# Performance work log

Measured on AMD Instinct MI355X. Metric: run time of the kernel, lower is better.

Reference implementation:

```python
import jax, jax.numpy as jnp
import numpy as np

B, I, H1, H2, E, T = 16384, 512, 256, 128, 8, 2


def setup_inputs() -> dict:
    key = jax.random.key(0)
    ks = jax.random.split(key, 4)
    # Xavier-ish scaling for stability
    x = jax.random.normal(ks[0], (B, I), dtype=jnp.float32)
    W1 = jax.random.normal(ks[1], (E, I, H1), dtype=jnp.float32) / np.sqrt(I)
    b1 = jnp.zeros((E, H1), dtype=jnp.float32)
    W2 = jax.random.normal(ks[2], (E, H1, H2), dtype=jnp.float32) / np.sqrt(H1)
    b2 = jnp.zeros((E, H2), dtype=jnp.float32)
    Wg = jax.random.normal(ks[3], (T, I, E), dtype=jnp.float32) / np.sqrt(I)
    bg = jnp.zeros((T, E), dtype=jnp.float32)
    return {"x": x, "W1": W1, "b1": b1, "W2": W2, "b2": b2, "Wg": Wg, "bg": bg}


def reference(x, W1, b1, W2, b2, Wg, bg):
    # All experts as one grouped GEMM: [E, B, H1]
    h = jax.nn.relu(jnp.einsum('bi,eih->ebh', x, W1) + b1[:, None, :])
    # Last expert layer (lastlayer_reg=True -> act applied): [E, B, H2]
    e_out = jax.nn.relu(jnp.einsum('ebh,eho->ebo', h, W2) + b2[:, None, :])
    # Per-task gates with softmax over experts: [T, B, E]
    gates = jax.nn.softmax(jnp.einsum('bi,tie->tbe', x, Wg) + bg[:, None, :], axis=-1)
    # Gate-weighted combine of expert outputs: [T, B, H2]
    towers = jnp.einsum('tbe,ebo->tbo', gates, e_out)
    return towers
```

## Files before the change

### kernel.cpp

```cpp
#include <hip/hip_runtime.h>
#include <hip/hip_bf16.h>

#define B_  16384
#define I_  512
#define H1_ 256
#define H2_ 128
#define E_  8
#define T_  2

typedef __attribute__((ext_vector_type(8))) short short8;
typedef __attribute__((ext_vector_type(4))) float float4_t;

__device__ inline unsigned short f2bf(float f) {
    union { float f; unsigned u; } v; v.f = f;
    unsigned r = v.u + 0x7FFFu + ((v.u >> 16) & 1u);
    return (unsigned short)(r >> 16);
}

__device__ inline void async_copy16(const unsigned short* g, unsigned short* l) {
    __builtin_amdgcn_global_load_lds(
        (const __attribute__((address_space(1))) void*)g,
        (__attribute__((address_space(3))) void*)l,
        16, 0, 0);
}

__global__ void prep_gates_kernel(const float* __restrict__ x,
                                  unsigned short* __restrict__ xb,
                                  const float* __restrict__ W1,
                                  unsigned short* __restrict__ w1t,
                                  const float* __restrict__ W2,
                                  unsigned short* __restrict__ w2t,
                                  const float* __restrict__ Wg,
                                  const float* __restrict__ bg,
                                  float* __restrict__ gates) {
    __shared__ __align__(16) char smem[16 * 520 * 2 + 4 * 16 * 16 * 4];
    int bid = blockIdx.x;
    int t = threadIdx.x;

    if (bid < 1024) {
        unsigned short* wgtL = (unsigned short*)smem;
        float (*red)[16][16] = (float (*)[16][16])(smem + 16 * 520 * 2);
#pragma unroll
        for (int j = 0; j < 32; ++j) {
            int idx = j * 256 + t;
            int e = idx & 7, i = (idx >> 3) & 511, task = idx >> 12;
            wgtL[(task * 8 + e) * 520 + i] = f2bf(Wg[idx]);
        }
        __syncthreads();

        int w = t >> 6, lane = t & 63;
        int col = lane & 15, quad = lane >> 4;
        int b0 = bid * 16;
        int k0 = w * 128;
        const float* xr = x + (size_t)(b0 + col) * I_ + k0 + quad * 8;
        unsigned short* xw = xb + (size_t)(b0 + col) * I_ + k0 + quad * 8;
        const unsigned short* bL = &wgtL[col * 520 + k0 + quad * 8];
        float4_t acc = {0.f, 0.f, 0.f, 0.f};
#pragma unroll
        for (int ks = 0; ks < 128; ks += 32) {
            float4_t xa = *(const float4_t*)(xr + ks);
            float4_t xc = *(const float4_t*)(xr + ks + 4);
            short8 a;
            a[0] = (short)f2bf(xa[0]); a[1] = (short)f2bf(xa[1]);
            a[2] = (short)f2bf(xa[2]); a[3] = (short)f2bf(xa[3]);
            a[4] = (short)f2bf(xc[0]); a[5] = (short)f2bf(xc[1]);
            a[6] = (short)f2bf(xc[2]); a[7] = (short)f2bf(xc[3]);
            *(short8*)(xw + ks) = a;
            short8 b = *(const short8*)(bL + ks);
            acc = __builtin_amdgcn_mfma_f32_16x16x32_bf16(a, b, acc, 0, 0, 0);
        }
#pragma unroll
        for (int p = 0; p < 4; ++p)
            red[w][quad * 4 + p][col] = acc[p];
        __syncthreads();
        int r = t >> 4, te = t & 15;
        float v = red[0][r][te] + red[1][r][te] + red[2][r][te] + red[3][r][te] + bg[te];
        float m = v;
        m = fmaxf(m, __shfl_xor(m, 1));
        m = fmaxf(m, __shfl_xor(m, 2));
        m = fmaxf(m, __shfl_xor(m, 4));
        float ev = __expf(v - m);
        float s = ev;
        s += __shfl_xor(s, 1);
        s += __shfl_xor(s, 2);
        s += __shfl_xor(s, 4);
        gates[(size_t)te * B_ + b0 + r] = ev / s;
    } else {
        float (*tile)[33] = (float (*)[33])smem;
        const float* in; unsigned short* outp; int R, C, e, r0, c0;
        if (bid < 2048) {
            int tl = bid - 1024;
            e = tl >> 7; int rem = tl & 127;
            R = I_; C = H1_;
            r0 = (rem >> 3) * 32; c0 = (rem & 7) * 32;
            in = W1; outp = w1t;
        } else {
            int tl = bid - 2048;
            e = tl >> 5; int rem = tl & 31;
            R = H1_; C = H2_;
            r0 = (rem >> 2) * 32; c0 = (rem & 3) * 32;
            in = W2; outp = w2t;
        }
        const float* inp = in + (size_t)e * R * C;
        unsigned short* op = outp + (size_t)e * R * C;
        int tx = t & 31, ty = t >> 5;
#pragma unroll
        for (int j = 0; j < 32; j += 8)
            tile[ty + j][tx] = inp[(size_t)(r0 + ty + j) * C + c0 + tx];
        __syncthreads();
#pragma unroll
        for (int j = 0; j < 32; j += 8)
            op[(size_t)(c0 + ty + j) * R + r0 + tx] = f2bf(tile[tx][ty + j]);
    }
}

__global__ __launch_bounds__(512, 2)
void l1_gemm_kernel(const unsigned short* __restrict__ xb,
                    const unsigned short* __restrict__ w1t,
                    const float* __restrict__ b1,
                    unsigned short* __restrict__ h) {
    __shared__ __align__(16) unsigned short smem[65536];

    int bid = blockIdx.x;
    int wg = (bid & 7) * 64 + (bid >> 3);
    int m0 = (wg >> 3) * 256;
    int e  = wg & 7;

    int t = threadIdx.x, w = t >> 6, lane = t & 63;
    int col = lane & 15, quad = lane >> 4;
    int wm = (w & 1) * 128;
    int wn = (w >> 1) * 64;

    int rowA = t >> 3;
    int csw  = ((t & 7) ^ (rowA & 7)) * 8;
    const unsigned short* aG = xb  + (size_t)(m0 + rowA) * I_ + csw;
    const unsigned short* bG = w1t + ((size_t)e * H1_ + rowA) * I_ + csw;

    unsigned short* As = smem;
    unsigned short* Bs = smem + 32768;
    int ldsw = w * 512;

    float4_t acc[8][4];
#pragma unroll
    for (int mf = 0; mf < 8; ++mf)
#pragma unroll
        for (int nf = 0; nf < 4; ++nf)
            acc[mf][nf] = (float4_t){0.f, 0.f, 0.f, 0.f};

#pragma unroll
    for (int p = 0; p < 4; ++p) {
        async_copy16(aG + ((size_t)p * 64) * I_, As + p * 4096 + ldsw);
        async_copy16(bG + ((size_t)p * 64) * I_, Bs + p * 4096 + ldsw);
    }

#pragma unroll 1
    for (int kt = 0; kt < 8; ++kt) {
        const int cur = kt & 1;
        const unsigned short* Ac = As + cur * 16384;
        const unsigned short* Bc = Bs + cur * 16384;

        if (kt < 7) {
            unsigned short* An = As + (cur ^ 1) * 16384;
            unsigned short* Bn = Bs + (cur ^ 1) * 16384;
            const unsigned short* aN = aG + (size_t)(kt + 1) * 64;
            const unsigned short* bN = bG + (size_t)(kt + 1) * 64;
#pragma unroll
            for (int p = 0; p < 4; ++p) {
                async_copy16(aN + ((size_t)p * 64) * I_, An + p * 4096 + ldsw);
                async_copy16(bN + ((size_t)p * 64) * I_, Bn + p * 4096 + ldsw);
            }
            asm volatile("s_waitcnt vmcnt(8)" ::: "memory");
        } else {
            asm volatile("s_waitcnt vmcnt(0)" ::: "memory");
        }
        asm volatile("s_barrier" ::: "memory");

#pragma unroll
        for (int kq = 0; kq < 2; ++kq) {
            int q = kq * 4 + quad;
            short8 af[8], bfv[4];
#pragma unroll
            for (int mf = 0; mf < 8; ++mf) {
                int r = wm + mf * 16 + col;
                af[mf] = *(const short8*)&Ac[r * 64 + ((q ^ (r & 7)) << 3)];
            }
#pragma unroll
            for (int nf = 0; nf < 4; ++nf) {
                int n = wn + nf * 16 + col;
                bfv[nf] = *(const short8*)&Bc[n * 64 + ((q ^ (n & 7)) << 3)];
            }
            __builtin_amdgcn_s_setprio(1);
#pragma unroll
            for (int mf = 0; mf < 8; ++mf)
#pragma unroll
                for (int nf = 0; nf < 4; ++nf)
                    acc[mf][nf] = __builtin_amdgcn_mfma_f32_16x16x32_bf16(
                        af[mf], bfv[nf], acc[mf][nf], 0, 0, 0);
            __builtin_amdgcn_s_setprio(0);
        }
        asm volatile("s_barrier" ::: "memory");
    }

    unsigned short* Ct = smem;
    const float* bE = b1 + e * H1_;
#pragma unroll
    for (int half = 0; half < 2; ++half) {
        if ((w & 1) == half) {
#pragma unroll
            for (int mf = 0; mf < 8; ++mf) {
#pragma unroll
                for (int nf = 0; nf < 4; ++nf) {
                    int n = wn + nf * 16 + col;
                    float bv = bE[n];
#pragma unroll
                    for (int p2 = 0; p2 < 4; ++p2) {
                        float v = acc[mf][nf][p2] + bv;
                        v = v > 0.f ? v : 0.f;
                        Ct[(mf * 16 + quad * 4 + p2) * 264 + n] = f2bf(v);
                    }
                }
            }
        }
        __syncthreads();
        unsigned short* hrow = h + ((size_t)e * B_ + m0 + half * 128) * H1_;
#pragma unroll
        for (int j = 0; j < 8; ++j) {
            int idx = j * 512 + t;
            int row = idx >> 5, cc = idx & 31;
            short8 vv = *(const short8*)&Ct[row * 264 + cc * 8];
            *(short8*)&hrow[(size_t)row * H1_ + cc * 8] = vv;
        }
        __syncthreads();
    }
}

__global__ __launch_bounds__(512, 4)
void fused_l2_combine_kernel(const unsigned short* __restrict__ h,
                             const unsigned short* __restrict__ w2t,
                             const float* __restrict__ b2,
                             const float* __restrict__ gates,
                             float* __restrict__ out) {
    __shared__ __align__(16) unsigned short ring[36864];
    __shared__ float gL[16][64];

    unsigned short* Aslot = ring;
    unsigned short* Bslot = ring + 12288;

    int b0 = blockIdx.x * 64;
    int t = threadIdx.x, w = t >> 6, lane = t & 63;
    int col = lane & 15, quad = lane >> 4;
    int wm = (w & 1) * 32, wn = (w >> 1) * 32;

    if (t < 256) {
        int te = t >> 4, r4 = (t & 15) * 4;
        *(float4_t*)&gL[te][r4] = *(const float4_t*)&gates[(size_t)te * B_ + b0 + r4];
    }

    int rowA = t >> 3;
    int csw  = ((t & 7) ^ (rowA & 7)) * 8;
    int ldsw = w * 512;

    float4_t tw0[2][2], tw1[2][2];
#pragma unroll
    for (int mi = 0; mi < 2; ++mi)
#pragma unroll
        for (int ni = 0; ni < 2; ++ni) {
            tw0[mi][ni] = (float4_t){0.f, 0.f, 0.f, 0.f};
            tw1[mi][ni] = (float4_t){0.f, 0.f, 0.f, 0.f};
        }

    auto stage = [&](int cid, int slot) {
        int ee = cid >> 2, kc = cid & 3;
        const unsigned short* hE = h + ((size_t)ee * B_ + b0 + rowA) * H1_ + kc * 64 + csw;
        async_copy16(hE, Aslot + slot * 4096 + ldsw);
        const unsigned short* wE = w2t + ((size_t)ee * H2_ + rowA) * H1_ + kc * 64 + csw;
        async_copy16(wE, Bslot + slot * 8192 + ldsw);
        async_copy16(wE + (size_t)64 * H1_, Bslot + slot * 8192 + 4096 + ldsw);
    };

    stage(0, 0);

    float4_t acc[2][2];
    int rd = 0, wr = 1;
#pragma unroll 1
    for (int cid = 0; cid < 32; ++cid) {
        if (cid < 31) {
            stage(cid + 1, wr);
            asm volatile("s_waitcnt vmcnt(3)" ::: "memory");
        } else {
            asm volatile("s_waitcnt vmcnt(0)" ::: "memory");
        }
        asm volatile("s_barrier" ::: "memory");

        if ((cid & 3) == 0) {
#pragma unroll
            for (int mi = 0; mi < 2; ++mi)
#pragma unroll
                for (int ni = 0; ni < 2; ++ni)
                    acc[mi][ni] = (float4_t){0.f, 0.f, 0.f, 0.f};
        }
        const unsigned short* Ac = Aslot + rd * 4096;
        const unsigned short* Bc = Bslot + rd * 8192;
#pragma unroll
        for (int kq = 0; kq < 2; ++kq) {
            int q = kq * 4 + quad;
            short8 af[2], bfv[2];
#pragma unroll
            for (int mi = 0; mi < 2; ++mi) {
                int r = wm + mi * 16 + col;
                af[mi] = *(const short8*)&Ac[r * 64 + ((q ^ (r & 7)) << 3)];
            }
#pragma unroll
            for (int ni = 0; ni < 2; ++ni) {
                int n = wn + ni * 16 + col;
                bfv[ni] = *(const short8*)&Bc[n * 64 + ((q ^ (n & 7)) << 3)];
            }
            __builtin_amdgcn_s_setprio(1);
#pragma unroll
            for (int mi = 0; mi < 2; ++mi)
#pragma unroll
                for (int ni = 0; ni < 2; ++ni)
                    acc[mi][ni] = __builtin_amdgcn_mfma_f32_16x16x32_bf16(
                        af[mi], bfv[ni], acc[mi][ni], 0, 0, 0);
            __builtin_amdgcn_s_setprio(0);
        }

        if ((cid & 3) == 3) {
            int ee = cid >> 2;
#pragma unroll
            for (int ni = 0; ni < 2; ++ni) {
                float bv = b2[ee * H2_ + wn + ni * 16 + col];
#pragma unroll
                for (int mi = 0; mi < 2; ++mi) {
#pragma unroll
                    for (int p = 0; p < 4; ++p) {
                        int rloc = wm + mi * 16 + quad * 4 + p;
                        float v = acc[mi][ni][p] + bv;
                        v = v > 0.f ? v : 0.f;
                        tw0[mi][ni][p] += gL[ee][rloc] * v;
                        tw1[mi][ni][p] += gL[8 + ee][rloc] * v;
                    }
                }
            }
        }
        rd = (rd == 2) ? 0 : rd + 1;
        wr = (wr == 2) ? 0 : wr + 1;
    }

#pragma unroll
    for (int mi = 0; mi < 2; ++mi) {
#pragma unroll
        for (int ni = 0; ni < 2; ++ni) {
            int n = wn + ni * 16 + col;
#pragma unroll
            for (int p = 0; p < 4; ++p) {
                int r = b0 + wm + mi * 16 + quad * 4 + p;
                out[(size_t)r * H2_ + n] = tw0[mi][ni][p];
                out[(size_t)B_ * H2_ + (size_t)r * H2_ + n] = tw1[mi][ni][p];
            }
        }
    }
}

extern "C" void kernel_launch(void* const* d_in, const int* in_sizes, int n_in,
                              void* d_out, int out_size, void* d_ws, size_t ws_size,
                              hipStream_t stream) {
    const float* x  = (const float*)d_in[0];
    const float* W1 = (const float*)d_in[1];
    const float* b1 = (const float*)d_in[2];
    const float* W2 = (const float*)d_in[3];
    const float* b2 = (const float*)d_in[4];
    const float* Wg = (const float*)d_in[5];
    const float* bg = (const float*)d_in[6];
    float* out = (float*)d_out;

    char* ws = (char*)d_ws;
    unsigned short* xb    = (unsigned short*)(ws);
    unsigned short* w1t   = (unsigned short*)(ws + 16777216);
    unsigned short* w2t   = (unsigned short*)(ws + 18874368);
    float*          gates = (float*)(ws + 19398656);
    unsigned short* h     = (unsigned short*)(ws + 20447232);

    prep_gates_kernel<<<dim3(2304), 256, 0, stream>>>(x, xb, W1, w1t, W2, w2t, Wg, bg, gates);

    l1_gemm_kernel<<<dim3(512), 512, 0, stream>>>(xb, w1t, b1, h);

    fused_l2_combine_kernel<<<dim3(B_ / 64), 512, 0, stream>>>(h, w2t, b2, gates, out);
}
```

Before: 163.6 us.

## Restructure L1 GEMM main loop into quadrant-level ping-pong pipeline

```diff
diff --git a/kernel.cpp b/kernel.cpp
--- a/kernel.cpp
+++ b/kernel.cpp
@@ -23,6 +23,10 @@
         (__attribute__((address_space(3))) void*)l,
         16, 0, 0);
 }
+
+#define BAR()  asm volatile("s_barrier" ::: "memory")
+#define LGKM() do { asm volatile("s_waitcnt lgkmcnt(0)" ::: "memory"); \
+                    __builtin_amdgcn_sched_barrier(0); } while (0)
 
 __global__ void prep_gates_kernel(const float* __restrict__ x,
                                   unsigned short* __restrict__ xb,
@@ -131,14 +135,10 @@
     int wm = (w & 1) * 128;
     int wn = (w >> 1) * 64;
 
-    int rowA = t >> 3;
-    int csw  = ((t & 7) ^ (rowA & 7)) * 8;
-    const unsigned short* aG = xb  + (size_t)(m0 + rowA) * I_ + csw;
-    const unsigned short* bG = w1t + ((size_t)e * H1_ + rowA) * I_ + csw;
+    int cswT = ((t & 7) ^ ((t >> 3) & 7)) * 8;
 
     unsigned short* As = smem;
     unsigned short* Bs = smem + 32768;
-    int ldsw = w * 512;
 
     float4_t acc[8][4];
 #pragma unroll
@@ -147,58 +147,102 @@
         for (int nf = 0; nf < 4; ++nf)
             acc[mf][nf] = (float4_t){0.f, 0.f, 0.f, 0.f};
 
-#pragma unroll
-    for (int p = 0; p < 4; ++p) {
-        async_copy16(aG + ((size_t)p * 64) * I_, As + p * 4096 + ldsw);
-        async_copy16(bG + ((size_t)p * 64) * I_, Bs + p * 4096 + ldsw);
-    }
+    auto stageA = [&](int kt, int mq, int bsel) {
+#pragma unroll
+        for (int hh = 0; hh < 2; ++hh) {
+            int lr = mq * 128 + hh * 64 + (t >> 3);
+            int m  = ((lr >> 6) & 1) * 128 + ((lr >> 7) & 1) * 64 + (lr & 63);
+            async_copy16(xb + (size_t)(m0 + m) * I_ + kt * 64 + cswT,
+                         As + bsel * 16384 + lr * 64 + (t & 7) * 8);
+        }
+    };
+    auto stageB = [&](int kt, int nq, int bsel) {
+#pragma unroll
+        for (int hh = 0; hh < 2; ++hh) {
+            int lr = nq * 128 + hh * 64 + (t >> 3);
+            int n  = ((lr >> 6) & 1) * 128 + ((lr >> 5) & 1) * 64 + ((lr >> 7) & 1) * 32 + (lr & 31);
+            async_copy16(w1t + ((size_t)e * H1_ + n) * I_ + kt * 64 + cswT,
+                         Bs + bsel * 16384 + lr * 64 + (t & 7) * 8);
+        }
+    };
+    auto dsA = [&](int bsel, int mq, short8 af[4][2]) {
+#pragma unroll
+        for (int m2 = 0; m2 < 4; ++m2) {
+            int r  = wm + (mq * 4 + m2) * 16 + col;
+            int lr = ((r >> 6) & 1) * 128 + ((r >> 7) & 1) * 64 + (r & 63);
+#pragma unroll
+            for (int kq = 0; kq < 2; ++kq) {
+                int q = kq * 4 + quad;
+                af[m2][kq] = *(const short8*)&As[bsel * 16384 + lr * 64 + ((q ^ (r & 7)) << 3)];
+            }
+        }
+    };
+    auto dsB = [&](int bsel, int nq, short8 bf[2][2]) {
+#pragma unroll
+        for (int n2 = 0; n2 < 2; ++n2) {
+            int n  = wn + (nq * 2 + n2) * 16 + col;
+            int lr = ((n >> 5) & 1) * 128 + ((n >> 7) & 1) * 64 + ((n >> 6) & 1) * 32 + (n & 31);
+#pragma unroll
+            for (int kq = 0; kq < 2; ++kq) {
+                int q = kq * 4 + quad;
+                bf[n2][kq] = *(const short8*)&Bs[bsel * 16384 + lr * 64 + ((q ^ (n & 7)) << 3)];
+            }
+        }
+    };
+    auto mfmaQ = [&](short8 af[4][2], short8 bf[2][2], int mq, int nq) {
+        __builtin_amdgcn_s_setprio(1);
+#pragma unroll
+        for (int m2 = 0; m2 < 4; ++m2)
+#pragma unroll
+            for (int n2 = 0; n2 < 2; ++n2)
+#pragma unroll
+                for (int kq = 0; kq < 2; ++kq)
+                    acc[mq * 4 + m2][nq * 2 + n2] = __builtin_amdgcn_mfma_f32_16x16x32_bf16(
+                        af[m2][kq], bf[n2][kq], acc[mq * 4 + m2][nq * 2 + n2], 0, 0, 0);
+        __builtin_amdgcn_s_setprio(0);
+    };
+
+    stageA(0, 0, 0); stageA(0, 1, 0); stageB(0, 0, 0); stageB(0, 1, 0);
+    stageA(1, 0, 1); stageA(1, 1, 1); stageB(1, 1, 1);
+    asm volatile("s_waitcnt vmcnt(6)" ::: "memory");
+    BAR();
 
 #pragma unroll 1
-    for (int kt = 0; kt < 8; ++kt) {
-        const int cur = kt & 1;
-        const unsigned short* Ac = As + cur * 16384;
-        const unsigned short* Bc = Bs + cur * 16384;
-
-        if (kt < 7) {
-            unsigned short* An = As + (cur ^ 1) * 16384;
-            unsigned short* Bn = Bs + (cur ^ 1) * 16384;
-            const unsigned short* aN = aG + (size_t)(kt + 1) * 64;
-            const unsigned short* bN = bG + (size_t)(kt + 1) * 64;
-#pragma unroll
-            for (int p = 0; p < 4; ++p) {
-                async_copy16(aN + ((size_t)p * 64) * I_, An + p * 4096 + ldsw);
-                async_copy16(bN + ((size_t)p * 64) * I_, Bn + p * 4096 + ldsw);
-            }
-            asm volatile("s_waitcnt vmcnt(8)" ::: "memory");
+    for (int j = 0; j < 4; ++j) {
+        short8 af[4][2], bf[2][2];
+        const int u = 2 * j, v = 2 * j + 1;
+        dsA(0, 0, af); dsB(0, 0, bf);
+        stageB(v, 0, 1);
+        BAR(); LGKM(); mfmaQ(af, bf, 0, 0); BAR();
+        dsB(0, 1, bf);
+        if (j < 3) stageA(u + 2, 0, 0);
+        BAR(); LGKM(); mfmaQ(af, bf, 0, 1); BAR();
+        dsA(0, 1, af);
+        BAR(); LGKM(); mfmaQ(af, bf, 1, 1); BAR();
+        dsB(0, 0, bf);
+        if (j < 3) {
+            stageA(u + 2, 1, 0); stageB(u + 2, 1, 0);
+            asm volatile("s_waitcnt vmcnt(6)" ::: "memory");
         } else {
             asm volatile("s_waitcnt vmcnt(0)" ::: "memory");
         }
-        asm volatile("s_barrier" ::: "memory");
-
-#pragma unroll
-        for (int kq = 0; kq < 2; ++kq) {
-            int q = kq * 4 + quad;
-            short8 af[8], bfv[4];
-#pragma unroll
-            for (int mf = 0; mf < 8; ++mf) {
-                int r = wm + mf * 16 + col;
-                af[mf] = *(const short8*)&Ac[r * 64 + ((q ^ (r & 7)) << 3)];
-            }
-#pragma unroll
-            for (int nf = 0; nf < 4; ++nf) {
-                int n = wn + nf * 16 + col;
-                bfv[nf] = *(const short8*)&Bc[n * 64 + ((q ^ (n & 7)) << 3)];
-            }
-            __builtin_amdgcn_s_setprio(1);
-#pragma unroll
-            for (int mf = 0; mf < 8; ++mf)
-#pragma unroll
-                for (int nf = 0; nf < 4; ++nf)
-                    acc[mf][nf] = __builtin_amdgcn_mfma_f32_16x16x32_bf16(
-                        af[mf], bfv[nf], acc[mf][nf], 0, 0, 0);
-            __builtin_amdgcn_s_setprio(0);
-        }
-        asm volatile("s_barrier" ::: "memory");
+        BAR(); LGKM(); mfmaQ(af, bf, 1, 0); BAR();
+        dsA(1, 0, af); dsB(1, 0, bf);
+        if (j < 3) stageB(u + 2, 0, 0);
+        BAR(); LGKM(); mfmaQ(af, bf, 0, 0); BAR();
+        dsB(1, 1, bf);
+        if (j < 3) stageA(v + 2, 0, 1);
+        BAR(); LGKM(); mfmaQ(af, bf, 0, 1); BAR();
+        dsA(1, 1, af);
+        BAR(); LGKM(); mfmaQ(af, bf, 1, 1); BAR();
+        dsB(1, 0, bf);
+        if (j < 3) {
+            stageA(v + 2, 1, 1); stageB(v + 2, 1, 1);
+            asm volatile("s_waitcnt vmcnt(6)" ::: "memory");
+        } else {
+            asm volatile("s_waitcnt vmcnt(0)" ::: "memory");
+        }
+        BAR(); LGKM(); mfmaQ(af, bf, 1, 0); BAR();
     }
 
     unsigned short* Ct = smem;
```

New measurement: 166.4 us. About the same (+1.7%).
